# Optimization experiments

Measured on AMD Instinct MI355X. Metric: run time of the kernel, lower is better.

The kernel has to match this reference:

```python
import jax, jax.numpy as jnp
import numpy as np

USER_NUM = 100000
ITEM_NUM = 150000
N = USER_NUM + ITEM_NUM
EMB = 64
N_LAYERS = 3
PROTO = 2048
NNZ = 5000000


def setup_inputs() -> dict:
    key = jax.random.key(0)
    k1, k2, k3, k4, k5, k6, k7 = jax.random.split(key, 7)
    # xavier_uniform bound for [rows, EMB] matrices
    def xavier(k, rows, cols):
        bound = float(np.sqrt(6.0 / (rows + cols)))
        return jax.random.uniform(k, (rows, cols), jnp.float32, -bound, bound)
    user_emb = xavier(k1, USER_NUM, EMB)
    item_emb = xavier(k2, ITEM_NUM, EMB)
    user_prototypes = xavier(k3, PROTO, EMB)
    item_prototypes = xavier(k4, PROTO, EMB)
    # COO sparse normalized adjacency (values ~ 1/deg scale)
    adj_rows = jax.random.randint(k5, (NNZ,), 0, N, jnp.int32)
    adj_cols = jax.random.randint(k6, (NNZ,), 0, N, jnp.int32)
    adj_vals = jax.random.uniform(k7, (NNZ,), jnp.float32) * 0.05
    return {
        "user_emb": user_emb,
        "item_emb": item_emb,
        "user_prototypes": user_prototypes,
        "item_prototypes": item_prototypes,
        "adj_vals": adj_vals,
        "adj_rows": adj_rows,
        "adj_cols": adj_cols,
    }


def _spmm(vals, rows, cols, x):
    # y = A @ x for COO A: gather source rows, scale, scatter-add to dest rows
    msgs = x[cols] * vals[:, None]  # [nnz, D]
    return jax.ops.segment_sum(msgs, rows, num_segments=N)


def reference(user_emb, item_emb, user_prototypes, item_prototypes,
              adj_vals, adj_rows, adj_cols):
    ego = jnp.concatenate([user_emb, item_emb], axis=0)  # [N, D]
    ego0 = ego
    acc = ego  # fused running sum instead of stacking all layers
    for _ in range(N_LAYERS):
        ego = _spmm(adj_vals, adj_rows, adj_cols, ego)
        acc = acc + ego
    mean_emb = acc / jnp.asarray(N_LAYERS + 1, ego.dtype)
    user_all = mean_emb[:USER_NUM]
    item_all = mean_emb[USER_NUM:]
    user_cl = ego0[:USER_NUM]
    item_cl = ego0[USER_NUM:]
    return (user_all, item_all, user_cl, item_cl, user_prototypes, item_prototypes)
```

## Files before the change

### kernel.cpp

```cpp
#include <hip/hip_runtime.h>

#define USER_NUM 100000
#define ITEM_NUM 150000
#define NTOT     250000
#define EMB      64
#define NNZ      5000000
#define NROW_ELEMS (NTOT * EMB)
#define NCB      977
#define NSUP     62
#define NSB1     1024
#define T1       4884
#define G2       16
#define SCAP     6144
#define PROTO_ELEMS (2048 * 64)

typedef unsigned uu2 __attribute__((ext_vector_type(2)));
typedef float    ff2 __attribute__((ext_vector_type(2)));
typedef float    ff4 __attribute__((ext_vector_type(4)));

#if defined(__has_builtin)
#if __has_builtin(__builtin_amdgcn_cvt_pk_f32_fp8) && __has_builtin(__builtin_amdgcn_cvt_pk_fp8_f32)
#define HW_FP8 1
#endif
#endif
#ifndef HW_FP8
#define HW_FP8 0
#endif

__device__ __forceinline__ unsigned enc1(float x) {
    unsigned b = __float_as_uint(x);
    unsigned s = (b >> 24) & 0x80u;
    unsigned mag = b & 0x7FFFFFFFu;
    if (mag < 0x3C800000u) return s;
    mag += 0x000FFFFFu + ((mag >> 20) & 1u);
    unsigned u7 = (mag >> 20) - (120u << 3);
    return s | (u7 > 0x7Eu ? 0x7Eu : u7);
}
__device__ __forceinline__ float dec1(unsigned u) {
    unsigned em = u & 0x7Fu;
    float f = __uint_as_float((((u & 0x80u) << 24) | (em << 20)) + (120u << 23));
    return (em < 8u) ? 0.f : f;
}

__device__ __forceinline__ uu2 enc8(const float* a) {
    uu2 w;
#if HW_FP8
    int lo = 0, hi = 0;
    lo = __builtin_amdgcn_cvt_pk_fp8_f32(a[0], a[1], lo, false);
    lo = __builtin_amdgcn_cvt_pk_fp8_f32(a[2], a[3], lo, true);
    hi = __builtin_amdgcn_cvt_pk_fp8_f32(a[4], a[5], hi, false);
    hi = __builtin_amdgcn_cvt_pk_fp8_f32(a[6], a[7], hi, true);
    w.x = (unsigned)lo; w.y = (unsigned)hi;
#else
    w.x = enc1(a[0]) | (enc1(a[1]) << 8) | (enc1(a[2]) << 16) | (enc1(a[3]) << 24);
    w.y = enc1(a[4]) | (enc1(a[5]) << 8) | (enc1(a[6]) << 16) | (enc1(a[7]) << 24);
#endif
    return w;
}

__device__ __forceinline__ void acc8q(float* acc, float v, uu2 u) {
#if HW_FP8
    ff2 a = __builtin_amdgcn_cvt_pk_f32_fp8(u.x, false);
    ff2 b = __builtin_amdgcn_cvt_pk_f32_fp8(u.x, true);
    ff2 c = __builtin_amdgcn_cvt_pk_f32_fp8(u.y, false);
    ff2 d = __builtin_amdgcn_cvt_pk_f32_fp8(u.y, true);
    acc[0] += v * a.x; acc[1] += v * a.y; acc[2] += v * b.x; acc[3] += v * b.y;
    acc[4] += v * c.x; acc[5] += v * c.y; acc[6] += v * d.x; acc[7] += v * d.y;
#else
#pragma unroll
    for (int k = 0; k < 4; ++k) acc[k]     += v * dec1((u.x >> (8 * k)) & 0xFFu);
#pragma unroll
    for (int k = 0; k < 4; ++k) acc[4 + k] += v * dec1((u.y >> (8 * k)) & 0xFFu);
#endif
}

__device__ __forceinline__ void dec8(float* d, uu2 u) {
#if HW_FP8
    ff2 a = __builtin_amdgcn_cvt_pk_f32_fp8(u.x, false);
    ff2 b = __builtin_amdgcn_cvt_pk_f32_fp8(u.x, true);
    ff2 c = __builtin_amdgcn_cvt_pk_f32_fp8(u.y, false);
    ff2 dd = __builtin_amdgcn_cvt_pk_f32_fp8(u.y, true);
    d[0] = a.x; d[1] = a.y; d[2] = b.x; d[3] = b.y;
    d[4] = c.x; d[5] = c.y; d[6] = dd.x; d[7] = dd.y;
#else
#pragma unroll
    for (int k = 0; k < 4; ++k) d[k]     = dec1((u.x >> (8 * k)) & 0xFFu);
#pragma unroll
    for (int k = 0; k < 4; ++k) d[4 + k] = dec1((u.y >> (8 * k)) & 0xFFu);
#endif
}

#define SCALE_F   32768.0f
#define OUT_C     (0.25f / 32768.0f)
#define QSCALE    327680.0f
#define QSTEP     (1.0f / 327680.0f)

__global__ __launch_bounds__(256) void hist_kernel(const int* __restrict__ rows,
                                                   int* __restrict__ counts) {
    __shared__ int sh[NCB];
    for (int i = threadIdx.x; i < NCB; i += 256) sh[i] = 0;
    __syncthreads();
    int stride = gridDim.x * blockDim.x;
    const int4* rows4 = (const int4*)rows;
    for (int i = blockIdx.x * blockDim.x + threadIdx.x; i < NNZ / 4; i += stride) {
        int4 r = rows4[i];
        atomicAdd(&sh[r.x >> 8], 1);
        atomicAdd(&sh[r.y >> 8], 1);
        atomicAdd(&sh[r.z >> 8], 1);
        atomicAdd(&sh[r.w >> 8], 1);
    }
    __syncthreads();
    for (int i = threadIdx.x; i < NCB; i += 256)
        if (sh[i]) atomicAdd(&counts[i], sh[i]);
}

__global__ void scan_kernel(const int* __restrict__ counts, int* __restrict__ boffs,
                            int* __restrict__ bcursor, int* __restrict__ cursor1,
                            int* __restrict__ offs) {
    __shared__ int sm[1024];
    int t = threadIdx.x;
    int c = (t < NCB) ? counts[t] : 0;
    sm[t] = c; __syncthreads();
    for (int off = 1; off < 1024; off <<= 1) {
        int v = (t >= off) ? sm[t - off] : 0;
        __syncthreads();
        sm[t] += v;
        __syncthreads();
    }
    if (t < NCB) { boffs[t] = sm[t] - c; bcursor[t] = sm[t] - c; }
    if (t == 1023) { boffs[NCB] = sm[1023]; offs[NTOT] = sm[1023]; }
    if (t < NSUP) cursor1[t] = sm[16 * t] - counts[16 * t];
}

__global__ __launch_bounds__(256) void part1(
        const int* __restrict__ rows, const int* __restrict__ cols,
        const float* __restrict__ vals, int* __restrict__ cursor1,
        int* __restrict__ exA, ushort* __restrict__ valQ) {
    __shared__ int cnt[NSUP];
    __shared__ int base[NSUP];
    int t = threadIdx.x;
    int tb = blockIdx.x * T1;
    int n = NNZ - tb; if (n <= 0) return; if (n > T1) n = T1;
    if (t < NSUP) cnt[t] = 0;
    __syncthreads();
    for (int i = t * 4; i < n; i += 1024) {
        int4 r = *(const int4*)(rows + tb + i);
        atomicAdd(&cnt[r.x >> 12], 1);
        atomicAdd(&cnt[r.y >> 12], 1);
        atomicAdd(&cnt[r.z >> 12], 1);
        atomicAdd(&cnt[r.w >> 12], 1);
    }
    __syncthreads();
    if (t < NSUP) {
        int c = cnt[t];
        base[t] = c ? atomicAdd(&cursor1[t], c) : 0;
        cnt[t] = 0;
    }
    __syncthreads();
    for (int i = t; i < n; i += 256) {
        int r = rows[tb + i];
        int s = r >> 12;
        int rank = atomicAdd(&cnt[s], 1);
        int p = base[s] + rank;
        exA[p] = cols[tb + i] | ((r & 4095) << 18);
        int q = (int)(vals[tb + i] * QSCALE + 0.5f);
        valQ[p] = (ushort)(q > 16383 ? 16383 : q);
    }
}

__global__ __launch_bounds__(256) void part2(
        const int* __restrict__ boffs, int* __restrict__ bcursor,
        const int* __restrict__ exA, const ushort* __restrict__ valQ,
        int* __restrict__ exB, ushort* __restrict__ valQB) {
    __shared__ int cnt[16], base[16], cur[16];
    int b = blockIdx.x;
    int s = b >> 4, k = b & 15;
    int t = threadIdx.x;
    int sb0 = s * 16;
    int nsb = NCB - sb0; if (nsb > 16) nsb = 16;
    int beg = boffs[sb0];
    int end = boffs[sb0 + nsb];
    int n = end - beg;
    int chunk = (n + G2 - 1) / G2;
    int cb = beg + k * chunk;
    int ce = cb + chunk; if (ce > end) ce = end;
    if (cb >= ce) return;
    if (t < 16) cnt[t] = 0;
    __syncthreads();
    for (int i = cb + t; i < ce; i += 256)
        atomicAdd(&cnt[(exA[i] >> 26) & 15], 1);
    __syncthreads();
    if (t < 16) {
        int c = cnt[t];
        base[t] = c ? atomicAdd(&bcursor[sb0 + t], c) : 0;
        cur[t] = 0;
    }
    __syncthreads();
    for (int i = cb + t; i < ce; i += 256) {
        int ex = exA[i];
        int j = (ex >> 26) & 15;
        int rank = atomicAdd(&cur[j], 1);
        exB[base[j] + rank] = ex;
        valQB[base[j] + rank] = valQ[i];
    }
}

__global__ __launch_bounds__(256) void bucket_sort(const int* __restrict__ boffs,
                                                   const int* __restrict__ exB,
                                                   const ushort* __restrict__ valQB,
                                                   unsigned* __restrict__ epkF,
                                                   int* __restrict__ offs) {
    __shared__ int sx[SCAP];
    __shared__ ushort sv[SCAP];
    __shared__ int cnt[256];
    __shared__ int base[256];
    __shared__ int cur[256];
    int b = blockIdx.x, t = threadIdx.x;
    int beg = boffs[b], end = boffs[b + 1];
    int n = end - beg; if (n > SCAP) n = SCAP;
    cnt[t] = 0;
    __syncthreads();
    for (int i = t; i < n; i += 256) {
        int ex = exB[beg + i];
        sx[i] = ex;
        sv[i] = valQB[beg + i];
        atomicAdd(&cnt[(ex >> 18) & 0xFF], 1);
    }
    __syncthreads();
    int c = cnt[t];
    base[t] = c; __syncthreads();
    for (int off = 1; off < 256; off <<= 1) {
        int v = (t >= off) ? base[t - off] : 0;
        __syncthreads();
        base[t] += v;
        __syncthreads();
    }
    int mybase = beg + base[t] - c;
    cur[t] = mybase;
    int r = b * 256 + t;
    if (r < NTOT) offs[r] = mybase;
    __syncthreads();
    for (int i = t; i < n; i += 256) {
        int ex = sx[i];
        int lr = (ex >> 18) & 0xFF;
        int p = atomicAdd(&cur[lr], 1);
        epkF[p] = ((unsigned)ex & 0x3FFFFu) | ((unsigned)sv[i] << 18);
    }
}

__global__ __launch_bounds__(256) void convert_kernel(
        const float* __restrict__ ue, const float* __restrict__ ie,
        const float* __restrict__ up, const float* __restrict__ ip,
        uu2* __restrict__ xq, float* __restrict__ out) {
    const int NG = NROW_ELEMS / 8;
    int g = blockIdx.x * blockDim.x + threadIdx.x;
    if (g < NG) {
        int base = g * 8;
        const float* src = (base < USER_NUM * EMB) ? ue + base
                                                   : ie + (base - USER_NUM * EMB);
        ff4 a = __builtin_nontemporal_load((const ff4*)src);
        ff4 b = __builtin_nontemporal_load((const ff4*)src + 1);
        ff4* oc = (ff4*)(out + NROW_ELEMS + base);
        __builtin_nontemporal_store(a, oc);
        __builtin_nontemporal_store(b, oc + 1);
        float s[8] = {a.x * SCALE_F, a.y * SCALE_F, a.z * SCALE_F, a.w * SCALE_F,
                      b.x * SCALE_F, b.y * SCALE_F, b.z * SCALE_F, b.w * SCALE_F};
        uu2 w = enc8(s);
        __builtin_nontemporal_store(w, xq + g);
    } else {
        int pj = (g - NG) * 8;
        const float* src;
        float* dst;
        if (pj < PROTO_ELEMS) {
            src = up + pj; dst = out + 2 * NROW_ELEMS + pj;
        } else if (pj < 2 * PROTO_ELEMS) {
            src = ip + (pj - PROTO_ELEMS);
            dst = out + 2 * NROW_ELEMS + pj;
        } else return;
        ff4 a = __builtin_nontemporal_load((const ff4*)src);
        ff4 b = __builtin_nontemporal_load((const ff4*)src + 1);
        __builtin_nontemporal_store(a, (ff4*)dst);
        __builtin_nontemporal_store(b, (ff4*)dst + 1);
    }
}

template <int LAYER>
__global__ __launch_bounds__(256) void spmm_q(
        const uu2* __restrict__ src,
        const int* __restrict__ offs, const unsigned* __restrict__ epk,
        uu2* __restrict__ lq,
        const float* __restrict__ ue, const float* __restrict__ ie,
        const uu2* __restrict__ l1q, const uu2* __restrict__ l2q,
        float* __restrict__ out) {
    int t = blockIdx.x * blockDim.x + threadIdx.x;
    int r = t >> 3, l = t & 7;
    if (r >= NTOT) return;
    int beg = offs[r], end = offs[r + 1];
    float acc[8] = {0.f, 0.f, 0.f, 0.f, 0.f, 0.f, 0.f, 0.f};
    int j = beg;
    for (; j + 3 < end; j += 4) {
        unsigned e0 = __builtin_nontemporal_load(epk + j);
        unsigned e1 = __builtin_nontemporal_load(epk + j + 1);
        unsigned e2 = __builtin_nontemporal_load(epk + j + 2);
        unsigned e3 = __builtin_nontemporal_load(epk + j + 3);
        uu2 u0 = src[(e0 & 0x3FFFFu) * 8 + l];
        uu2 u1 = src[(e1 & 0x3FFFFu) * 8 + l];
        uu2 u2 = src[(e2 & 0x3FFFFu) * 8 + l];
        uu2 u3 = src[(e3 & 0x3FFFFu) * 8 + l];
        acc8q(acc, (float)(e0 >> 18) * QSTEP, u0);
        acc8q(acc, (float)(e1 >> 18) * QSTEP, u1);
        acc8q(acc, (float)(e2 >> 18) * QSTEP, u2);
        acc8q(acc, (float)(e3 >> 18) * QSTEP, u3);
    }
    for (; j < end; ++j) {
        unsigned e0 = __builtin_nontemporal_load(epk + j);
        uu2 u0 = src[(e0 & 0x3FFFFu) * 8 + l];
        acc8q(acc, (float)(e0 >> 18) * QSTEP, u0);
    }
    int idx = r * 8 + l;
    if (LAYER == 1 || LAYER == 2) {
        uu2 w = enc8(acc);
        __builtin_nontemporal_store(w, lq + idx);
    } else {
        int base = r * EMB + l * 8;
        const float* ep = (r < USER_NUM) ? ue + base
                                         : ie + (base - USER_NUM * EMB);
        ff4 ea = __builtin_nontemporal_load((const ff4*)ep);
        ff4 eb = __builtin_nontemporal_load((const ff4*)ep + 1);
        uu2 u1 = __builtin_nontemporal_load(l1q + idx);
        uu2 u2 = __builtin_nontemporal_load(l2q + idx);
        float d1[8], d2[8];
        dec8(d1, u1);
        dec8(d2, u2);
        ff4 o0, o1;
        o0.x = ea.x * 0.25f + (d1[0] + d2[0] + acc[0]) * OUT_C;
        o0.y = ea.y * 0.25f + (d1[1] + d2[1] + acc[1]) * OUT_C;
        o0.z = ea.z * 0.25f + (d1[2] + d2[2] + acc[2]) * OUT_C;
        o0.w = ea.w * 0.25f + (d1[3] + d2[3] + acc[3]) * OUT_C;
        o1.x = eb.x * 0.25f + (d1[4] + d2[4] + acc[4]) * OUT_C;
        o1.y = eb.y * 0.25f + (d1[5] + d2[5] + acc[5]) * OUT_C;
        o1.z = eb.z * 0.25f + (d1[6] + d2[6] + acc[6]) * OUT_C;
        o1.w = eb.w * 0.25f + (d1[7] + d2[7] + acc[7]) * OUT_C;
        __builtin_nontemporal_store(o0, (ff4*)(out + base));
        __builtin_nontemporal_store(o1, (ff4*)(out + base) + 1);
    }
}

extern "C" void kernel_launch(void* const* d_in, const int* in_sizes, int n_in,
                              void* d_out, int out_size, void* d_ws, size_t ws_size,
                              hipStream_t stream) {
    const float* ue   = (const float*)d_in[0];
    const float* ie   = (const float*)d_in[1];
    const float* up   = (const float*)d_in[2];
    const float* ip   = (const float*)d_in[3];
    const float* vals = (const float*)d_in[4];
    const int*   rows = (const int*)d_in[5];
    const int*   cols = (const int*)d_in[6];
    float* out = (float*)d_out;

    int*      exA    = (int*)d_ws;
    int*      exB    = (int*)d_ws + 5000000;
    ushort*   valQ   = (ushort*)((int*)d_ws + 10000000);
    ushort*   valQB  = (ushort*)((int*)d_ws + 11250000);
    unsigned* epkF   = (unsigned*)((int*)d_ws + 12500000);
    uu2*      xq     = (uu2*)((int*)d_ws + 17500000);
    uu2*      l1q    = (uu2*)((int*)d_ws + 21500000);
    int*      offs   = (int*)d_ws + 26000000;
    int*      boffs  = (int*)d_ws + 26250112;
    int*      bcursor= (int*)d_ws + 26252000;
    int*      bcounts= (int*)d_ws + 26253000;
    int*      cursor1= (int*)d_ws + 26254000;
    uu2*      l2q    = xq;

    const int sgrid = (NTOT * 8 + 255) / 256;
    const int cgrid = (NROW_ELEMS / 8 + 2 * PROTO_ELEMS / 8 + 255) / 256;

    hipMemsetAsync(bcounts, 0, NCB * sizeof(int), stream);
    hist_kernel<<<256, 256, 0, stream>>>(rows, bcounts);
    scan_kernel<<<1, 1024, 0, stream>>>(bcounts, boffs, bcursor, cursor1, offs);
    part1      <<<NSB1, 256, 0, stream>>>(rows, cols, vals, cursor1, exA, valQ);
    part2      <<<NSUP * G2, 256, 0, stream>>>(boffs, bcursor, exA, valQ, exB, valQB);
    bucket_sort<<<NCB, 256, 0, stream>>>(boffs, exB, valQB, epkF, offs);

    convert_kernel<<<cgrid, 256, 0, stream>>>(ue, ie, up, ip, xq, out);

    spmm_q<1><<<sgrid, 256, 0, stream>>>(xq,  offs, epkF, l1q,
                                         nullptr, nullptr, nullptr, nullptr, nullptr);
    spmm_q<2><<<sgrid, 256, 0, stream>>>(l1q, offs, epkF, l2q,
                                         nullptr, nullptr, nullptr, nullptr, nullptr);
    spmm_q<3><<<sgrid, 256, 0, stream>>>(l2q, offs, epkF, nullptr,
                                         ue, ie, l1q, l2q, out);
}
```

Before: 474.3 us.

## Sort each row's edges by column index in bucket_sort for gather locality

The packed edge word now puts the column index in the high bits and the quantized value in the low 14 bits. bucket_sort builds each row's segment in shared memory, insertion-sorts it per thread so columns are ascending, then writes the block out with coalesced nontemporal stores. Sorted columns are meant to improve cache locality of the source-row gathers in spmm and make the epk writes contiguous. The costs are a serial per-thread insertion sort in the preprocessing kernel, more shared memory, and quantized values limited to 14 bits.

```diff
diff --git a/kernel.cpp b/kernel.cpp
--- a/kernel.cpp
+++ b/kernel.cpp
@@ -210,10 +210,11 @@
                                                    const ushort* __restrict__ valQB,
                                                    unsigned* __restrict__ epkF,
                                                    int* __restrict__ offs) {
-    __shared__ int sx[SCAP];
-    __shared__ ushort sv[SCAP];
+    __shared__ unsigned sw[SCAP];
+    __shared__ unsigned char slr[SCAP];
+    __shared__ unsigned sg[SCAP];
     __shared__ int cnt[256];
-    __shared__ int base[256];
+    __shared__ int lbase[256];
     __shared__ int cur[256];
     int b = blockIdx.x, t = threadIdx.x;
     int beg = boffs[b], end = boffs[b + 1];
@@ -222,30 +223,41 @@
     __syncthreads();
     for (int i = t; i < n; i += 256) {
         int ex = exB[beg + i];
-        sx[i] = ex;
-        sv[i] = valQB[beg + i];
-        atomicAdd(&cnt[(ex >> 18) & 0xFF], 1);
+        unsigned q = valQB[beg + i];
+        int lr = (ex >> 18) & 0xFF;
+        sw[i] = ((unsigned)(ex & 0x3FFFF) << 14) | q;
+        slr[i] = (unsigned char)lr;
+        atomicAdd(&cnt[lr], 1);
     }
     __syncthreads();
     int c = cnt[t];
-    base[t] = c; __syncthreads();
+    lbase[t] = c; __syncthreads();
     for (int off = 1; off < 256; off <<= 1) {
-        int v = (t >= off) ? base[t - off] : 0;
+        int v = (t >= off) ? lbase[t - off] : 0;
         __syncthreads();
-        base[t] += v;
+        lbase[t] += v;
         __syncthreads();
     }
-    int mybase = beg + base[t] - c;
-    cur[t] = mybase;
+    int myb = lbase[t] - c;
+    cur[t] = myb;
     int r = b * 256 + t;
-    if (r < NTOT) offs[r] = mybase;
+    if (r < NTOT) offs[r] = beg + myb;
     __syncthreads();
     for (int i = t; i < n; i += 256) {
-        int ex = sx[i];
-        int lr = (ex >> 18) & 0xFF;
+        int lr = slr[i];
         int p = atomicAdd(&cur[lr], 1);
-        epkF[p] = ((unsigned)ex & 0x3FFFFu) | ((unsigned)sv[i] << 18);
-    }
+        sg[p] = sw[i];
+    }
+    __syncthreads();
+    for (int i = myb + 1; i < myb + c; ++i) {
+        unsigned key = sg[i];
+        int j = i - 1;
+        while (j >= myb && sg[j] > key) { sg[j + 1] = sg[j]; --j; }
+        sg[j + 1] = key;
+    }
+    __syncthreads();
+    for (int i = t; i < n; i += 256)
+        __builtin_nontemporal_store(sg[i], epkF + beg + i);
 }
 
 __global__ __launch_bounds__(256) void convert_kernel(
@@ -303,19 +315,19 @@
         unsigned e1 = __builtin_nontemporal_load(epk + j + 1);
         unsigned e2 = __builtin_nontemporal_load(epk + j + 2);
         unsigned e3 = __builtin_nontemporal_load(epk + j + 3);
-        uu2 u0 = src[(e0 & 0x3FFFFu) * 8 + l];
-        uu2 u1 = src[(e1 & 0x3FFFFu) * 8 + l];
-        uu2 u2 = src[(e2 & 0x3FFFFu) * 8 + l];
-        uu2 u3 = src[(e3 & 0x3FFFFu) * 8 + l];
-        acc8q(acc, (float)(e0 >> 18) * QSTEP, u0);
-        acc8q(acc, (float)(e1 >> 18) * QSTEP, u1);
-        acc8q(acc, (float)(e2 >> 18) * QSTEP, u2);
-        acc8q(acc, (float)(e3 >> 18) * QSTEP, u3);
+        uu2 u0 = src[(e0 >> 14) * 8 + l];
+        uu2 u1 = src[(e1 >> 14) * 8 + l];
+        uu2 u2 = src[(e2 >> 14) * 8 + l];
+        uu2 u3 = src[(e3 >> 14) * 8 + l];
+        acc8q(acc, (float)(e0 & 0x3FFFu) * QSTEP, u0);
+        acc8q(acc, (float)(e1 & 0x3FFFu) * QSTEP, u1);
+        acc8q(acc, (float)(e2 & 0x3FFFu) * QSTEP, u2);
+        acc8q(acc, (float)(e3 & 0x3FFFu) * QSTEP, u3);
     }
     for (; j < end; ++j) {
         unsigned e0 = __builtin_nontemporal_load(epk + j);
-        uu2 u0 = src[(e0 & 0x3FFFFu) * 8 + l];
-        acc8q(acc, (float)(e0 >> 18) * QSTEP, u0);
+        uu2 u0 = src[(e0 >> 14) * 8 + l];
+        acc8q(acc, (float)(e0 & 0x3FFFu) * QSTEP, u0);
     }
     int idx = r * 8 + l;
     if (LAYER == 1 || LAYER == 2) {
```

Measured after the change: 571.1 us. 20.4% more time.
